# Performance work log

Measured on AMD Instinct MI355X. Metric: run time of the kernel, lower is better.

The kernel has to match this reference:

```python
import jax, jax.numpy as jnp
import numpy as np

N_HEAD = 16
SCALE = True
NEG = 10000.0


def setup_inputs() -> dict:
    key = jax.random.key(0)
    ks = jax.random.split(key, 5)
    B, S, D = 4, 1024, 1024
    x = jax.random.normal(ks[0], (B, S, D), dtype=jnp.float32)
    # GPT-2 Conv1D weights: W has shape [in, out], init ~N(0, 0.02)
    w_attn = jax.random.normal(ks[1], (D, 3 * D), dtype=jnp.float32) * 0.02
    b_attn = jnp.zeros((3 * D,), dtype=jnp.float32)
    w_proj = jax.random.normal(ks[2], (D, D), dtype=jnp.float32) * 0.02
    b_proj = jnp.zeros((D,), dtype=jnp.float32)
    return {"x": x, "w_attn": w_attn, "b_attn": b_attn,
            "w_proj": w_proj, "b_proj": b_proj}


def reference(x, w_attn, b_attn, w_proj, b_proj):
    B, S, D = x.shape
    H = N_HEAD
    hd = D // H
    # c_attn: Conv1D == x @ W + b
    qkv = jnp.einsum('bsd,de->bse', x, w_attn) + b_attn
    q, k, v = jnp.split(qkv, 3, axis=-1)
    # split heads -> [B, H, S, hd]
    q = q.reshape(B, S, H, hd).transpose(0, 2, 1, 3)
    k = k.reshape(B, S, H, hd).transpose(0, 2, 1, 3)
    v = v.reshape(B, S, H, hd).transpose(0, 2, 1, 3)
    # scores [B, H, S, S]
    w = jnp.einsum('bhqd,bhkd->bhqk', q, k)
    if SCALE:
        w = w / jnp.sqrt(jnp.float32(hd))
    # multiplicative causal mask: w*b - 10000*(1-b)
    bmask = jnp.tril(jnp.ones((S, S), dtype=w.dtype))[None, None]
    w = w * bmask - NEG * (1.0 - bmask)
    w = jax.nn.softmax(w, axis=-1)
    # attn_pdrop = 0 -> dropout is identity
    a = jnp.einsum('bhqk,bhkd->bhqd', w, v)
    # merge heads
    a = a.transpose(0, 2, 1, 3).reshape(B, S, D)
    # c_proj; resid_pdrop = 0
    out = jnp.einsum('bsd,de->bse', a, w_proj) + b_proj
    return out
```

## Files before the change

### kernel.cpp

```cpp
#include <hip/hip_runtime.h>
#include <hip/hip_bf16.h>


typedef __bf16 bf16x8 __attribute__((ext_vector_type(8)));
typedef float f32x4 __attribute__((ext_vector_type(4)));

__device__ __forceinline__ void load_lds16(const void* g, void* l) {
  __builtin_amdgcn_global_load_lds(
      (const __attribute__((address_space(1))) void*)g,
      (__attribute__((address_space(3))) void*)l, 16, 0, 0);
}

__global__ __launch_bounds__(256) void prep(
    const float* __restrict__ x, const float* __restrict__ w_attn,
    const float* __restrict__ w_proj, __bf16* __restrict__ Xb,
    __bf16* __restrict__ WT_attn, __bf16* __restrict__ WT_proj) {
  __shared__ __bf16 tile[32][33];
  const int blk = blockIdx.x;
  const int tid = threadIdx.x;
  if (blk < 4096) {
    const float* W;
    __bf16* WT;
    int n0, k0, N;
    if (blk < 3072) {
      W = w_attn; WT = WT_attn; N = 3072;
      n0 = (blk % 96) * 32; k0 = (blk / 96) * 32;
    } else {
      W = w_proj; WT = WT_proj; N = 1024;
      const int t = blk - 3072;
      n0 = (t & 31) * 32; k0 = (t >> 5) * 32;
    }
    const int tx = tid & 31, ty = tid >> 5;
#pragma unroll
    for (int j = 0; j < 32; j += 8)
      tile[ty + j][tx] = (__bf16)W[(size_t)(k0 + ty + j) * N + n0 + tx];
    __syncthreads();
#pragma unroll
    for (int j = 0; j < 32; j += 8)
      WT[(size_t)(n0 + ty + j) * 1024 + k0 + tx] = tile[tx][ty + j];
  } else {
    const size_t i = (size_t)(blk - 4096) * 4096 + tid * 16;
    const float4* xp = (const float4*)(x + i);
    float4 a = xp[0], b = xp[1], c = xp[2], d = xp[3];
    bf16x8 o0, o1;
    o0[0] = (__bf16)a.x; o0[1] = (__bf16)a.y; o0[2] = (__bf16)a.z; o0[3] = (__bf16)a.w;
    o0[4] = (__bf16)b.x; o0[5] = (__bf16)b.y; o0[6] = (__bf16)b.z; o0[7] = (__bf16)b.w;
    o1[0] = (__bf16)c.x; o1[1] = (__bf16)c.y; o1[2] = (__bf16)c.z; o1[3] = (__bf16)c.w;
    o1[4] = (__bf16)d.x; o1[5] = (__bf16)d.y; o1[6] = (__bf16)d.z; o1[7] = (__bf16)d.w;
    *(bf16x8*)(Xb + i) = o0;
    *(bf16x8*)(Xb + i + 8) = o1;
  }
}

__global__ __launch_bounds__(256) void transpose_v(
    const __bf16* __restrict__ Vr, __bf16* __restrict__ VT) {
  const int lane = threadIdx.x & 63, wave = threadIdx.x >> 6;
  const int bh = blockIdx.x >> 4;
  const int kb = (blockIdx.x & 15) * 64;
  const int b = bh >> 4, h = bh & 15;
  const __bf16* src =
      Vr + (size_t)(b * 1024 + kb + lane) * 1024 + h * 64 + wave * 16;
  bf16x8 v0 = *(const bf16x8*)src;
  bf16x8 v1 = *(const bf16x8*)(src + 8);
  __bf16* dst = VT + ((size_t)bh * 64 + wave * 16) * 1024 + kb + lane;
#pragma unroll
  for (int i = 0; i < 8; ++i) {
    dst[(size_t)i * 1024] = v0[i];
    dst[(size_t)(i + 8) * 1024] = v1[i];
  }
}

#define GEMM_CORE(A_, BT_, K_)                                                   \
  __shared__ __bf16 sA[128 * 32];                                               \
  __shared__ __bf16 sB[128 * 32];                                               \
  const int tid = threadIdx.x;                                                  \
  const int lane = tid & 63;                                                    \
  const int wave = tid >> 6;                                                    \
  const int waveM = wave >> 1, waveN = wave & 1;                                \
  const int quad = lane >> 4;                                                   \
  const int l16 = lane & 15;                                                    \
  const int rowBase = blockIdx.y * 128;                                         \
  const int colBase = blockIdx.x * 128;                                         \
  const int rIn = lane >> 2;                                                    \
  const int sIn = lane & 3;                                                     \
  const int gc = sIn ^ (rIn & 3) ^ ((rIn >> 2) & 3);                            \
  const int readSlot = quad ^ (l16 & 3) ^ ((l16 >> 2) & 3);                     \
  f32x4 acc[4][4] = {};                                                         \
  for (int k0 = 0; k0 < K_; k0 += 32) {                                         \
    __syncthreads();                                                            \
    _Pragma("unroll") for (int j = 0; j < 2; ++j) {                             \
      const int rb = wave * 32 + j * 16;                                        \
      load_lds16(&A_[(size_t)(rowBase + rb + rIn) * K_ + k0 + gc * 8],          \
                 &sA[rb * 32]);                                                 \
      load_lds16(&BT_[(size_t)(colBase + rb + rIn) * K_ + k0 + gc * 8],         \
                 &sB[rb * 32]);                                                 \
    }                                                                           \
    __syncthreads();                                                            \
    bf16x8 af[4], bfr[4];                                                       \
    _Pragma("unroll") for (int mt = 0; mt < 4; ++mt)                            \
      af[mt] = *(const bf16x8*)(&sA[(waveM * 64 + mt * 16 + l16) * 32 +         \
                                    readSlot * 8]);                             \
    _Pragma("unroll") for (int nt = 0; nt < 4; ++nt)                            \
      bfr[nt] = *(const bf16x8*)(&sB[(waveN * 64 + nt * 16 + l16) * 32 +        \
                                     readSlot * 8]);                            \
    _Pragma("unroll") for (int mt = 0; mt < 4; ++mt)                            \
    _Pragma("unroll") for (int nt = 0; nt < 4; ++nt)                            \
      acc[mt][nt] = __builtin_amdgcn_mfma_f32_16x16x32_bf16(                    \
          af[mt], bfr[nt], acc[mt][nt], 0, 0, 0);                               \
  }


#define BAR8 asm volatile("s_barrier" ::: "memory")
#define LGKM0 asm volatile("s_waitcnt lgkmcnt(0)" ::: "memory")

#define STG(GMAT, GROW0, K0, LOFF)                                             \
  _Pragma("unroll") for (int i_ = 0; i_ < 2; ++i_)                             \
    load_lds16((GMAT) + (size_t)((GROW0) + i_ * 64 + wave * 8 + srow) * 1024 + \
                   (K0) + schunk * 8,                                          \
               smem8 + (LOFF) + (i_ * 64 + wave * 8) * 64);

#define LDA8(BASE, MH)                                                         \
  _Pragma("unroll") for (int m_ = 0; m_ < 4; ++m_)                             \
  _Pragma("unroll") for (int kk_ = 0; kk_ < 2; ++kk_)                          \
    af[m_][kk_] = *(const bf16x8*)((BASE) + ((MH)*64 + m_ * 16 + l16) * 64 +   \
                                   (((kk_ * 4 + quad) ^ rsw) * 8));

#define LDB8(BASE, NLO)                                                        \
  _Pragma("unroll") for (int n_ = 0; n_ < 2; ++n_)                             \
  _Pragma("unroll") for (int kk_ = 0; kk_ < 2; ++kk_)                          \
    bf[(NLO) + n_][kk_] =                                                      \
        *(const bf16x8*)((BASE) + ((waveN & 1) * 64 + ((NLO) + n_) * 16 +      \
                                   l16) * 64 +                                 \
                         (((kk_ * 4 + quad) ^ rsw) * 8));

#define MFMA_HALF(MH, NLO)                                                     \
  __builtin_amdgcn_s_setprio(1);                                               \
  _Pragma("unroll") for (int m_ = 0; m_ < 4; ++m_)                             \
  _Pragma("unroll") for (int n_ = 0; n_ < 2; ++n_) {                           \
    acc[(MH)*4 + m_][(NLO) + n_] = __builtin_amdgcn_mfma_f32_16x16x32_bf16(    \
        af[m_][0], bf[(NLO) + n_][0], acc[(MH)*4 + m_][(NLO) + n_], 0, 0, 0);  \
    acc[(MH)*4 + m_][(NLO) + n_] = __builtin_amdgcn_mfma_f32_16x16x32_bf16(    \
        af[m_][1], bf[(NLO) + n_][1], acc[(MH)*4 + m_][(NLO) + n_], 0, 0, 0);  \
  }                                                                            \
  __builtin_amdgcn_s_setprio(0);

__global__ __launch_bounds__(512, 2) void gemm_qkv8(
    const __bf16* __restrict__ A, const __bf16* __restrict__ BT,
    const float* __restrict__ bias, __bf16* __restrict__ Qp,
    __bf16* __restrict__ Kp, __bf16* __restrict__ Vr) {
  __shared__ __bf16 smem8[65536];
  const int tid = threadIdx.x;
  const int lane = tid & 63;
  const int wave = tid >> 6;
  const int waveM = wave >> 2;
  const int waveN = wave & 3;
  const int l16 = lane & 15;
  const int quad = lane >> 4;
  const int rsw = l16 & 7;
  const int srow = lane >> 3;
  const int schunk = (lane & 7) ^ srow;

  const int bid = blockIdx.x;
  const int swz = (bid & 7) * 24 + (bid >> 3);
  const int tm = swz / 12, tn = swz - (swz / 12) * 12;
  const int rowBase = tm * 256;
  const int colBase = tn * 256;

  const __bf16* aRd = smem8 + waveM * 8192;
  const __bf16* bRd = smem8 + 16384 + (waveN >> 1) * 8192;

  f32x4 acc[8][4] = {};
  bf16x8 af[4][2], bf[4][2];

  STG(A, rowBase, 0, 0);
  STG(A, rowBase + 128, 0, 8192);
  STG(BT, colBase, 0, 16384);
  STG(BT, colBase + 128, 0, 24576);
  STG(BT, colBase, 64, 32768 + 16384);
  STG(BT, colBase + 128, 64, 32768 + 24576);
  STG(A, rowBase, 64, 32768);
  asm volatile("s_waitcnt vmcnt(6)" ::: "memory");
  BAR8;

  for (int t = 0; t < 8; ++t) {
    const int kO = t * 128 + 64;
    const int kS2 = t * 128 + 128;
    const int kS3 = t * 128 + 192;
    const bool s2 = kS2 < 1024;
    const bool s3 = kS3 < 1024;

    LDA8(aRd, 0);
    LDB8(bRd, 0);
    STG(A, rowBase + 128, kO, 32768 + 8192);
    BAR8; LGKM0;
    MFMA_HALF(0, 0);
    BAR8;

    LDB8(bRd, 2);
    BAR8; LGKM0;
    MFMA_HALF(0, 2);
    BAR8;

    LDA8(aRd, 1);
    if (s2) { STG(BT, colBase, kS2, 16384); }
    BAR8; LGKM0;
    MFMA_HALF(1, 2);
    BAR8;

    if (s2) {
      STG(BT, colBase + 128, kS2, 24576);
      STG(A, rowBase, kS2, 0);
      asm volatile("s_waitcnt vmcnt(6)" ::: "memory");
    } else {
      asm volatile("s_waitcnt vmcnt(0)" ::: "memory");
    }
    BAR8;
    MFMA_HALF(1, 0);
    BAR8;

    LDA8(aRd + 32768, 0);
    LDB8(bRd + 32768, 0);
    if (s2) { STG(A, rowBase + 128, kS2, 8192); }
    BAR8; LGKM0;
    MFMA_HALF(0, 0);
    BAR8;

    LDB8(bRd + 32768, 2);
    BAR8; LGKM0;
    MFMA_HALF(0, 2);
    BAR8;

    LDA8(aRd + 32768, 1);
    if (s3) { STG(BT, colBase, kS3, 32768 + 16384); }
    BAR8; LGKM0;
    MFMA_HALF(1, 2);
    BAR8;

    if (s3) {
      STG(BT, colBase + 128, kS3, 32768 + 24576);
      STG(A, rowBase, kS3, 32768);
    }
    asm volatile("s_waitcnt vmcnt(6)" ::: "memory");
    BAR8;
    MFMA_HALF(1, 0);
    BAR8;
  }

  const int seg = colBase >> 10;
#pragma unroll
  for (int mm = 0; mm < 8; ++mm) {
    const int row0 = rowBase + waveM * 128 + mm * 16 + quad * 4;
#pragma unroll
    for (int n = 0; n < 4; ++n) {
      const int col = colBase + waveN * 64 + n * 16 + l16;
      const float bv = bias[col];
      const int cc = col & 1023;
#pragma unroll
      for (int r = 0; r < 4; ++r) {
        const int row = row0 + r;
        const float v = acc[mm][n][r] + bv;
        if (seg == 2) {
          Vr[(size_t)row * 1024 + cc] = (__bf16)v;
        } else {
          const int bh = ((row >> 10) << 4) + (cc >> 6);
          __bf16* dst = (seg == 0) ? Qp : Kp;
          dst[((size_t)bh << 16) + (size_t)(row & 1023) * 64 + (cc & 63)] =
              (__bf16)v;
        }
      }
    }
  }
}

__global__ __launch_bounds__(256) void gemm_out(
    const __bf16* __restrict__ A, const __bf16* __restrict__ BT,
    const float* __restrict__ bias, float* __restrict__ C) {
  GEMM_CORE(A, BT, 1024)
#pragma unroll
  for (int mt = 0; mt < 4; ++mt) {
    const int row = rowBase + waveM * 64 + mt * 16 + quad * 4;
#pragma unroll
    for (int nt = 0; nt < 4; ++nt) {
      const int col = colBase + waveN * 64 + nt * 16 + l16;
      const float bv = bias[col];
#pragma unroll
      for (int r = 0; r < 4; ++r)
        C[(size_t)(row + r) * 1024 + col] = acc[mt][nt][r] + bv;
    }
  }
}

__global__ __launch_bounds__(256) void attn_mfma(
    const __bf16* __restrict__ Qp, const __bf16* __restrict__ Kp,
    const __bf16* __restrict__ VT, __bf16* __restrict__ Aout) {
  __shared__ __bf16 sK[128 * 64];
  __shared__ __bf16 sV[64 * 128];
  __shared__ __bf16 sP[4 * 16 * 128];

  const int tid = threadIdx.x;
  const int lane = tid & 63;
  const int wave = tid >> 6;
  const int quad = lane >> 4;
  const int l16 = lane & 15;
  const int swq = l16 & 7;

  const int bh = blockIdx.x >> 3;
  const int pr = blockIdx.x & 7;
  const int b = bh >> 4, h = bh & 15;
  const int qbA = pr * 64, qbB = (15 - pr) * 64;
  const int ktA_max = pr >> 1, ktB_max = (15 - pr) >> 1;

  const __bf16* Qb = Qp + ((size_t)bh << 16);
  const __bf16* Kb = Kp + ((size_t)bh << 16);
  const __bf16* VTb = VT + (size_t)bh * 64 * 1024;

  bf16x8 qA0A, qA1A, qA0B, qA1B;
  {
    const __bf16* qr = Qb + (size_t)(qbA + wave * 16 + l16) * 64 + quad * 8;
    qA0A = *(const bf16x8*)qr;
    qA1A = *(const bf16x8*)(qr + 32);
    qr = Qb + (size_t)(qbB + wave * 16 + l16) * 64 + quad * 8;
    qA0B = *(const bf16x8*)qr;
    qA1B = *(const bf16x8*)(qr + 32);
  }

  f32x4 OA[4] = {}, OB[4] = {};
  float psA[4] = {0.f, 0.f, 0.f, 0.f}, psB[4] = {0.f, 0.f, 0.f, 0.f};
  __bf16* pw = sP + wave * 2048;

  for (int kt = 0; kt <= ktB_max; ++kt) {
    const int kb = kt * 128;
    __syncthreads();

#pragma unroll
    for (int i = 0; i < 4; ++i) {
      const int rb = wave * 32 + i * 8;
      load_lds16(Kb + (size_t)(kb + rb + (lane >> 3)) * 64 +
                     (((lane & 7) ^ ((lane >> 3) & 7)) << 3),
                 &sK[rb * 64]);
    }
#pragma unroll
    for (int i = 0; i < 4; ++i) {
      const int db = wave * 16 + i * 4;
      const int d = db + (lane >> 4);
      load_lds16(VTb + (size_t)d * 1024 + kb + (((lane & 15) ^ (d & 7)) << 3),
                 &sV[db * 128]);
    }
    __syncthreads();

    {
      float sc[8][4];
#pragma unroll
      for (int n = 0; n < 8; ++n) {
        const int key = n * 16 + l16;
        bf16x8 kB0 = *(const bf16x8*)(&sK[key * 64 + ((quad ^ swq) << 3)]);
        bf16x8 kB1 = *(const bf16x8*)(&sK[key * 64 + (((quad + 4) ^ swq) << 3)]);
        f32x4 c = {};
        c = __builtin_amdgcn_mfma_f32_16x16x32_bf16(qA0B, kB0, c, 0, 0, 0);
        c = __builtin_amdgcn_mfma_f32_16x16x32_bf16(qA1B, kB1, c, 0, 0, 0);
#pragma unroll
        for (int r = 0; r < 4; ++r) sc[n][r] = c[r] * 0.125f;
      }
      if (kt == ktB_max) {
#pragma unroll
        for (int n = 0; n < 8; ++n) {
          const int kg = kb + n * 16 + l16;
#pragma unroll
          for (int r = 0; r < 4; ++r)
            if (kg > qbB + wave * 16 + quad * 4 + r) sc[n][r] = -1.0e30f;
        }
      }
#pragma unroll
      for (int n = 0; n < 8; ++n)
#pragma unroll
        for (int r = 0; r < 4; ++r) {
          float p = __expf(fminf(sc[n][r], 60.0f));
          sc[n][r] = p;
          psB[r] += p;
        }
      {
        const int kb8 = l16 >> 3, lo = l16 & 7;
#pragma unroll
        for (int n = 0; n < 8; ++n) {
          const int chunk = n * 2 + kb8;
#pragma unroll
          for (int r = 0; r < 4; ++r) {
            const int q = quad * 4 + r;
            pw[q * 128 + ((chunk ^ (q & 7)) << 3) + lo] = (__bf16)sc[n][r];
          }
        }
      }
#pragma unroll
      for (int cc = 0; cc < 4; ++cc) {
        bf16x8 pA = *(const bf16x8*)(&pw[l16 * 128 + (((cc * 4 + quad) ^ swq) << 3)]);
#pragma unroll
        for (int nt = 0; nt < 4; ++nt) {
          bf16x8 vB = *(const bf16x8*)(&sV[(nt * 16 + l16) * 128 +
                                           (((cc * 4 + quad) ^ swq) << 3)]);
          OB[nt] = __builtin_amdgcn_mfma_f32_16x16x32_bf16(pA, vB, OB[nt], 0, 0, 0);
        }
      }
    }

    if (kt <= ktA_max) {
      float sc[8][4];
#pragma unroll
      for (int n = 0; n < 8; ++n) {
        const int key = n * 16 + l16;
        bf16x8 kB0 = *(const bf16x8*)(&sK[key * 64 + ((quad ^ swq) << 3)]);
        bf16x8 kB1 = *(const bf16x8*)(&sK[key * 64 + (((quad + 4) ^ swq) << 3)]);
        f32x4 c = {};
        c = __builtin_amdgcn_mfma_f32_16x16x32_bf16(qA0A, kB0, c, 0, 0, 0);
        c = __builtin_amdgcn_mfma_f32_16x16x32_bf16(qA1A, kB1, c, 0, 0, 0);
#pragma unroll
        for (int r = 0; r < 4; ++r) sc[n][r] = c[r] * 0.125f;
      }
      if (kt == ktA_max) {
#pragma unroll
        for (int n = 0; n < 8; ++n) {
          const int kg = kb + n * 16 + l16;
#pragma unroll
          for (int r = 0; r < 4; ++r)
            if (kg > qbA + wave * 16 + quad * 4 + r) sc[n][r] = -1.0e30f;
        }
      }
#pragma unroll
      for (int n = 0; n < 8; ++n)
#pragma unroll
        for (int r = 0; r < 4; ++r) {
          float p = __expf(fminf(sc[n][r], 60.0f));
          sc[n][r] = p;
          psA[r] += p;
        }
      {
        const int kb8 = l16 >> 3, lo = l16 & 7;
#pragma unroll
        for (int n = 0; n < 8; ++n) {
          const int chunk = n * 2 + kb8;
#pragma unroll
          for (int r = 0; r < 4; ++r) {
            const int q = quad * 4 + r;
            pw[q * 128 + ((chunk ^ (q & 7)) << 3) + lo] = (__bf16)sc[n][r];
          }
        }
      }
#pragma unroll
      for (int cc = 0; cc < 4; ++cc) {
        bf16x8 pA = *(const bf16x8*)(&pw[l16 * 128 + (((cc * 4 + quad) ^ swq) << 3)]);
#pragma unroll
        for (int nt = 0; nt < 4; ++nt) {
          bf16x8 vB = *(const bf16x8*)(&sV[(nt * 16 + l16) * 128 +
                                           (((cc * 4 + quad) ^ swq) << 3)]);
          OA[nt] = __builtin_amdgcn_mfma_f32_16x16x32_bf16(pA, vB, OA[nt], 0, 0, 0);
        }
      }
    }
  }

  float invA[4], invB[4];
#pragma unroll
  for (int r = 0; r < 4; ++r) {
    float pa = psA[r], pb = psB[r];
    pa += __shfl_xor(pa, 1); pb += __shfl_xor(pb, 1);
    pa += __shfl_xor(pa, 2); pb += __shfl_xor(pb, 2);
    pa += __shfl_xor(pa, 4); pb += __shfl_xor(pb, 4);
    pa += __shfl_xor(pa, 8); pb += __shfl_xor(pb, 8);
    invA[r] = 1.0f / pa;
    invB[r] = 1.0f / pb;
  }
#pragma unroll
  for (int nt = 0; nt < 4; ++nt) {
#pragma unroll
    for (int r = 0; r < 4; ++r) {
      const int qA = qbA + wave * 16 + quad * 4 + r;
      const int qB = qbB + wave * 16 + quad * 4 + r;
      Aout[((size_t)b * 1024 + qA) * 1024 + h * 64 + nt * 16 + l16] =
          (__bf16)(OA[nt][r] * invA[r]);
      Aout[((size_t)b * 1024 + qB) * 1024 + h * 64 + nt * 16 + l16] =
          (__bf16)(OB[nt][r] * invB[r]);
    }
  }
}

extern "C" void kernel_launch(void* const* d_in, const int* in_sizes, int n_in,
                              void* d_out, int out_size, void* d_ws,
                              size_t ws_size, hipStream_t stream) {
  const float* x      = (const float*)d_in[0];
  const float* w_attn = (const float*)d_in[1];
  const float* b_attn = (const float*)d_in[2];
  const float* w_proj = (const float*)d_in[3];
  const float* b_proj = (const float*)d_in[4];
  float* out = (float*)d_out;

  char* ws = (char*)d_ws;
  __bf16* WT_attn = (__bf16*)(ws);
  __bf16* WT_proj = (__bf16*)(ws + 6291456);
  __bf16* Xb      = (__bf16*)(ws + 8388608);
  __bf16* Qp      = (__bf16*)(ws + 16777216);
  __bf16* Kp      = (__bf16*)(ws + 25165824);
  __bf16* Vr      = (__bf16*)(ws + 33554432);
  __bf16* Aattn   = (__bf16*)(ws + 41943040);
  __bf16* VT      = Xb;

  prep<<<5120, 256, 0, stream>>>(x, w_attn, w_proj, Xb, WT_attn, WT_proj);
  gemm_qkv8<<<192, 512, 0, stream>>>(Xb, WT_attn, b_attn, Qp, Kp, Vr);
  transpose_v<<<1024, 256, 0, stream>>>(Vr, VT);
  attn_mfma<<<512, 256, 0, stream>>>(Qp, Kp, VT, Aattn);
  gemm_out<<<dim3(8, 32), 256, 0, stream>>>(Aattn, WT_proj, b_proj, out);
}
```

Baseline: 178.9 us.

## Fuse V transpose into QKV GEMM epilogue via swizzled LDS staging

Removes the separate transpose_v kernel by having the QKV GEMM write the V segment directly in transposed [B,H,hd,S] layout. The V tile is staged through shared memory with an XOR swizzle, then written out as 16-byte vectors along the sequence dimension. This drops one kernel launch and a full read/write pass over V. The cost is an extra barrier and LDS round trip in the GEMM epilogue for the V-producing blocks.

```diff
diff --git a/kernel.cpp b/kernel.cpp
--- a/kernel.cpp
+++ b/kernel.cpp
@@ -3,6 +3,7 @@
 
 
 typedef __bf16 bf16x8 __attribute__((ext_vector_type(8)));
+typedef __bf16 bf16x4 __attribute__((ext_vector_type(4)));
 typedef float f32x4 __attribute__((ext_vector_type(4)));
 
 __device__ __forceinline__ void load_lds16(const void* g, void* l) {
@@ -49,24 +50,6 @@
     o1[4] = (__bf16)d.x; o1[5] = (__bf16)d.y; o1[6] = (__bf16)d.z; o1[7] = (__bf16)d.w;
     *(bf16x8*)(Xb + i) = o0;
     *(bf16x8*)(Xb + i + 8) = o1;
-  }
-}
-
-__global__ __launch_bounds__(256) void transpose_v(
-    const __bf16* __restrict__ Vr, __bf16* __restrict__ VT) {
-  const int lane = threadIdx.x & 63, wave = threadIdx.x >> 6;
-  const int bh = blockIdx.x >> 4;
-  const int kb = (blockIdx.x & 15) * 64;
-  const int b = bh >> 4, h = bh & 15;
-  const __bf16* src =
-      Vr + (size_t)(b * 1024 + kb + lane) * 1024 + h * 64 + wave * 16;
-  bf16x8 v0 = *(const bf16x8*)src;
-  bf16x8 v1 = *(const bf16x8*)(src + 8);
-  __bf16* dst = VT + ((size_t)bh * 64 + wave * 16) * 1024 + kb + lane;
-#pragma unroll
-  for (int i = 0; i < 8; ++i) {
-    dst[(size_t)i * 1024] = v0[i];
-    dst[(size_t)(i + 8) * 1024] = v1[i];
   }
 }
 
@@ -147,7 +130,7 @@
 __global__ __launch_bounds__(512, 2) void gemm_qkv8(
     const __bf16* __restrict__ A, const __bf16* __restrict__ BT,
     const float* __restrict__ bias, __bf16* __restrict__ Qp,
-    __bf16* __restrict__ Kp, __bf16* __restrict__ Vr) {
+    __bf16* __restrict__ Kp, __bf16* __restrict__ Vt) {
   __shared__ __bf16 smem8[65536];
   const int tid = threadIdx.x;
   const int lane = tid & 63;
@@ -247,23 +230,48 @@
   }
 
   const int seg = colBase >> 10;
-#pragma unroll
-  for (int mm = 0; mm < 8; ++mm) {
-    const int row0 = rowBase + waveM * 128 + mm * 16 + quad * 4;
-#pragma unroll
-    for (int n = 0; n < 4; ++n) {
-      const int col = colBase + waveN * 64 + n * 16 + l16;
-      const float bv = bias[col];
-      const int cc = col & 1023;
-#pragma unroll
-      for (int r = 0; r < 4; ++r) {
-        const int row = row0 + r;
-        const float v = acc[mm][n][r] + bv;
-        if (seg == 2) {
-          Vr[(size_t)row * 1024 + cc] = (__bf16)v;
-        } else {
+  if (seg == 2) {
+#pragma unroll
+    for (int mm = 0; mm < 8; ++mm) {
+      const int r0 = waveM * 128 + mm * 16 + quad * 4;
+#pragma unroll
+      for (int n = 0; n < 4; ++n) {
+        const int cR = waveN * 64 + n * 16 + l16;
+        const float bv = bias[colBase + cR];
+        bf16x4 pk;
+#pragma unroll
+        for (int r = 0; r < 4; ++r) pk[r] = (__bf16)(acc[mm][n][r] + bv);
+        *(bf16x4*)(&smem8[cR * 256 + (r0 ^ (l16 << 4))]) = pk;
+      }
+    }
+    __syncthreads();
+    const int b_ = rowBase >> 10;
+    const int s0 = rowBase & 1023;
+    const int hBase = (colBase & 1023) >> 6;
+    const int ch = lane & 31;
+#pragma unroll
+    for (int p = 0; p < 16; ++p) {
+      const int c = p * 16 + wave * 2 + (lane >> 5);
+      bf16x8 v =
+          *(const bf16x8*)(&smem8[c * 256 + ((ch * 8) ^ ((c & 15) << 4))]);
+      const int bhd = (b_ * 16 + hBase + (c >> 6)) * 64 + (c & 63);
+      *(bf16x8*)(&Vt[(size_t)bhd * 1024 + s0 + ch * 8]) = v;
+    }
+  } else {
+#pragma unroll
+    for (int mm = 0; mm < 8; ++mm) {
+      const int row0 = rowBase + waveM * 128 + mm * 16 + quad * 4;
+#pragma unroll
+      for (int n = 0; n < 4; ++n) {
+        const int col = colBase + waveN * 64 + n * 16 + l16;
+        const float bv = bias[col];
+        const int cc = col & 1023;
+        __bf16* dst = (seg == 0) ? Qp : Kp;
+#pragma unroll
+        for (int r = 0; r < 4; ++r) {
+          const int row = row0 + r;
+          const float v = acc[mm][n][r] + bv;
           const int bh = ((row >> 10) << 4) + (cc >> 6);
-          __bf16* dst = (seg == 0) ? Qp : Kp;
           dst[((size_t)bh << 16) + (size_t)(row & 1023) * 64 + (cc & 63)] =
               (__bf16)v;
         }
@@ -498,13 +506,11 @@
   __bf16* Xb      = (__bf16*)(ws + 8388608);
   __bf16* Qp      = (__bf16*)(ws + 16777216);
   __bf16* Kp      = (__bf16*)(ws + 25165824);
-  __bf16* Vr      = (__bf16*)(ws + 33554432);
+  __bf16* VT      = (__bf16*)(ws + 33554432);
   __bf16* Aattn   = (__bf16*)(ws + 41943040);
-  __bf16* VT      = Xb;
 
   prep<<<5120, 256, 0, stream>>>(x, w_attn, w_proj, Xb, WT_attn, WT_proj);
-  gemm_qkv8<<<192, 512, 0, stream>>>(Xb, WT_attn, b_attn, Qp, Kp, Vr);
-  transpose_v<<<1024, 256, 0, stream>>>(Vr, VT);
+  gemm_qkv8<<<192, 512, 0, stream>>>(Xb, WT_attn, b_attn, Qp, Kp, VT);
   attn_mfma<<<512, 256, 0, stream>>>(Qp, Kp, VT, Aattn);
   gemm_out<<<dim3(8, 32), 256, 0, stream>>>(Aattn, WT_proj, b_proj, out);
 }
```

New measurement: 171.7 us. 4.0% less time.
